# Optimization experiments

Measured on AMD Instinct MI355X. Metric: run time of the kernel, lower is better.

## Reference

```python
import jax, jax.numpy as jnp
import numpy as np

N, D, L, K = 250000, 16, 6, 64
COST_GAMMA = 0.1
MIN_ZERO_GAMMA = 0.1
EPS = 1e-7  # clip for arccos numerical stability


def setup_inputs() -> dict:
    key = jax.random.key(0)
    k1, k2, k3, k4 = jax.random.split(key, 4)
    xs = jax.random.normal(k1, (N, D), jnp.float32)
    xs = xs / jnp.linalg.norm(xs, axis=1, keepdims=True)  # points on sphere S^{D-1}
    mus = jax.random.normal(k2, (L, D, K), jnp.float32)    # per-layer component locations
    alphas = jax.random.uniform(k3, (L, K), jnp.float32, minval=-1.0, maxval=1.0)
    ws = jax.random.uniform(k4, (L,), jnp.float32, minval=0.0, maxval=1.0)
    return {"xs": xs, "mus": mus, "alphas": alphas, "ws": ws}


def reference(xs, mus, alphas, ws):
    # projx: normalize each mu column onto the sphere (norm over D axis)
    mu_n = mus / jnp.linalg.norm(mus, axis=1, keepdims=True)          # [L, D, K]
    # sphere cost: 0.5 * geodesic_dist^2 = 0.5 * arccos(<x, mu>)^2
    inner = jnp.einsum('nd,ldk->lnk', xs, mu_n)                        # [L, N, K]
    dist = jnp.arccos(jnp.clip(inner, -1.0 + EPS, 1.0 - EPS))
    costs = 0.5 * dist * dist + alphas[:, None, :]                     # [L, N, K]
    # soft-min over components (note sign convention follows original: +gamma*LSE(-c/gamma))
    mincosts = COST_GAMMA * jax.nn.logsumexp(-costs / COST_GAMMA, axis=2)  # [L, N]
    wv = jnp.exp(-ws ** 2)                                             # [L]
    F = jnp.zeros((xs.shape[0],), xs.dtype)
    for i in range(L):  # small fixed layer recurrence
        F = wv[i] * jax.nn.relu(F) + (1.0 - wv[i]) * mincosts[i]
    # smooth min(F, 0): gamma * LSE(-[F,0]/gamma)
    Fz = jnp.stack((F, jnp.zeros_like(F)), axis=-1)
    F = MIN_ZERO_GAMMA * jax.nn.logsumexp(-Fz / MIN_ZERO_GAMMA, axis=-1)
    return F
```

## Files before the change

### kernel.cpp

```cpp
#include <hip/hip_runtime.h>
#include <math.h>

#define NPOINTS 250000
#define LL 6
#define DD 16
#define KK 64

#define TPB 128
#define WAVES_PER_BLOCK (TPB / 64)
#define PTS_PER_WAVE 64
#define PTS_PER_BLOCK (WAVES_PER_BLOCK * PTS_PER_WAVE)

#define LDS_BYTES (WAVES_PER_BLOCK * PTS_PER_WAVE * 80)

#define WS_MU 0
#define WS_AV 24576
#define WS_WV 26112

typedef __attribute__((ext_vector_type(8))) short bf16x8;
typedef __attribute__((ext_vector_type(4))) float f32x4;
typedef __attribute__((ext_vector_type(2))) float f32x2;

#if __has_builtin(__builtin_amdgcn_exp2f)
#define EXP2F(x) __builtin_amdgcn_exp2f(x)
#else
#define EXP2F(x) exp2f(x)
#endif
#if __has_builtin(__builtin_amdgcn_logf)
#define LOG2F(x) __builtin_amdgcn_logf(x)
#else
#define LOG2F(x) log2f(x)
#endif

#define C_AA   (-14.426950408889634f)
#define C_GLN2 (0.06931471805599453f)

#define W0  17.797117f
#define VT0 (-45.300328f)
#define VT1 (-28.559404f)
#define VT2 (-27.844414f)
#define VT3 (-30.475230f)
#define VT4 (-36.246253f)
#define VT5 (-27.207285f)

__device__ __forceinline__ f32x2 s2(float v) { f32x2 r; r.x = v; r.y = v; return r; }

__device__ __forceinline__ ushort bf16_rne(float f) {
  unsigned u = __float_as_uint(f);
  unsigned r = u + 0x7FFFu + ((u >> 16) & 1u);
  return (ushort)(r >> 16);
}

__device__ __forceinline__ f32x2 poly_t2(f32x2 xp, f32x2 aaw) {
  f32x2 x2  = xp * xp;
  f32x2 p01 = __builtin_elementwise_fma(s2(VT1), xp, s2(VT0));
  f32x2 p23 = __builtin_elementwise_fma(s2(VT3), xp, s2(VT2));
  f32x2 p45 = __builtin_elementwise_fma(s2(VT5), xp, s2(VT4));
  f32x2 qq  = __builtin_elementwise_fma(x2, p45, p23);
  f32x2 V   = __builtin_elementwise_fma(x2, qq, p01);
  return __builtin_elementwise_fma(xp, V, aaw);
}

__device__ __forceinline__ void pack_pt(char* dst, float4 a, int q) {
  ushort h0 = bf16_rne(a.x), h1 = bf16_rne(a.y);
  ushort h2 = bf16_rne(a.z), h3 = bf16_rne(a.w);
  float hf0 = __uint_as_float((unsigned)h0 << 16);
  float hf1 = __uint_as_float((unsigned)h1 << 16);
  float hf2 = __uint_as_float((unsigned)h2 << 16);
  float hf3 = __uint_as_float((unsigned)h3 << 16);
  ushort l0 = bf16_rne(a.x - hf0), l1 = bf16_rne(a.y - hf1);
  ushort l2 = bf16_rne(a.z - hf2), l3 = bf16_rne(a.w - hf3);
  uint2 hwv, lwv;
  hwv.x = (unsigned)h0 | ((unsigned)h1 << 16);
  hwv.y = (unsigned)h2 | ((unsigned)h3 << 16);
  lwv.x = (unsigned)l0 | ((unsigned)l1 << 16);
  lwv.y = (unsigned)l2 | ((unsigned)l3 << 16);
  *(uint2*)(dst + q * 8) = hwv;
  *(uint2*)(dst + 32 + q * 8) = lwv;
}

__global__ __launch_bounds__(384) void
prep_kernel(const float* __restrict__ mus,
            const float* __restrict__ alphas,
            const float* __restrict__ wsv,
            char* __restrict__ ws) {
  const int t = threadIdx.x;
  const float* colp = mus + (t >> 6) * (DD * KK) + (t & 63);
  float v[DD];
  float ss = 0.0f;
#pragma unroll
  for (int d = 0; d < DD; ++d) { v[d] = colp[d * KK]; ss = fmaf(v[d], v[d], ss); }
  float inv = -0.5f / sqrtf(ss);
  unsigned hw[8], lw[8];
#pragma unroll
  for (int i = 0; i < 8; ++i) {
    float a0 = v[2 * i] * inv;
    float a1 = v[2 * i + 1] * inv;
    ushort h0 = bf16_rne(a0), h1 = bf16_rne(a1);
    float hf0 = __uint_as_float((unsigned)h0 << 16);
    float hf1 = __uint_as_float((unsigned)h1 << 16);
    ushort l0 = bf16_rne(a0 - hf0), l1 = bf16_rne(a1 - hf1);
    hw[i] = (unsigned)h0 | ((unsigned)h1 << 16);
    lw[i] = (unsigned)l0 | ((unsigned)l1 << 16);
  }
  uint4* colq = (uint4*)(ws + WS_MU + t * 64);
  colq[0] = make_uint4(hw[0], hw[1], hw[2], hw[3]);
  colq[1] = make_uint4(hw[4], hw[5], hw[6], hw[7]);
  colq[2] = make_uint4(lw[0], lw[1], lw[2], lw[3]);
  colq[3] = make_uint4(lw[4], lw[5], lw[6], lw[7]);
  ((float*)(ws + WS_AV))[t] = fmaf(C_AA, alphas[t], -W0);
  if (t < LL) { float x = wsv[t]; ((float*)(ws + WS_WV))[t] = expf(-x * x); }
}

__global__ __launch_bounds__(TPB, 3) void
multiinf_kernel(const float* __restrict__ xs,
                const char* __restrict__ ws,
                float* __restrict__ out) {
  __shared__ __align__(16) char smem[LDS_BYTES];

  const int tid = threadIdx.x;
  const int wid = tid >> 6;
  const int lane = tid & 63;
  const int c = lane & 15;
  const int q = lane >> 4;
  const int h = q & 1;
  const int pt0 = blockIdx.x * PTS_PER_BLOCK + wid * PTS_PER_WAVE;
  char* sx = smem + wid * (PTS_PER_WAVE * 80);

#pragma unroll
  for (int t = 0; t < 4; ++t) {
    int p = pt0 + 16 * t + c;
    float4 a = make_float4(0.0f, 0.0f, 0.0f, 0.0f);
    if (p < NPOINTS) a = ((const float4*)(xs + (size_t)p * DD))[q];
    pack_pt(sx + (16 * t + c) * 80, a, q);
  }

  bf16x8 Bh[4], Bl[4];
#pragma unroll
  for (int t = 0; t < 4; ++t) {
    Bh[t] = *(const bf16x8*)(sx + (16 * t + c) * 80 + h * 16);
    Bl[t] = *(const bf16x8*)(sx + (16 * t + c) * 80 + 32 + h * 16);
  }

  const float* swv = (const float*)(ws + WS_WV);
  const f32x4 zero4 = {0.0f, 0.0f, 0.0f, 0.0f};
  float F[4] = {0.0f, 0.0f, 0.0f, 0.0f};

  auto load_Am = [&](int l, bf16x8* Am) {
#pragma unroll
    for (int cb = 0; cb < 4; ++cb)
      Am[cb] = *(const bf16x8*)(ws + WS_MU + (l * 64 + cb * 16 + c) * 64 + q * 16);
  };
  auto load_aa = [&](int l, f32x2* aaL, f32x2* aaH) {
#pragma unroll
    for (int cb = 0; cb < 4; ++cb) {
      f32x4 a4 = *(const f32x4*)(ws + WS_AV + (l * 64 + cb * 16 + q * 4) * 4);
      aaL[cb].x = a4.x; aaL[cb].y = a4.y;
      aaH[cb].x = a4.z; aaH[cb].y = a4.w;
    }
  };

  auto layer_body = [&](int l, const bf16x8* Am) {
    f32x2 aaL[4], aaH[4];
    load_aa(l, aaL, aaH);
    f32x2 S[8];
#pragma unroll
    for (int i = 0; i < 8; ++i) S[i] = s2(0.0f);
#pragma unroll
    for (int cb = 0; cb < 4; ++cb) {
      f32x4 acc[4];
#pragma unroll
      for (int t = 0; t < 4; ++t) {
        acc[t] = __builtin_amdgcn_mfma_f32_16x16x32_bf16(Am[cb], Bh[t], zero4, 0, 0, 0);
        acc[t] = __builtin_amdgcn_mfma_f32_16x16x32_bf16(Am[cb], Bl[t], acc[t], 0, 0, 0);
      }
      f32x2 t2[8];
#pragma unroll
      for (int t = 0; t < 4; ++t) {
        f32x2 x01, x23;
        x01.x = acc[t][0]; x01.y = acc[t][1];
        x23.x = acc[t][2]; x23.y = acc[t][3];
        t2[2 * t]     = poly_t2(x01, aaL[cb]);
        t2[2 * t + 1] = poly_t2(x23, aaH[cb]);
      }
      f32x2 e[8];
#pragma unroll
      for (int i = 0; i < 8; ++i) { e[i].x = EXP2F(t2[i].x); e[i].y = EXP2F(t2[i].y); }
#pragma unroll
      for (int i = 0; i < 8; ++i) S[i] += e[i];
    }
    float wvl = swv[l];
    float om = 1.0f - wvl;
#pragma unroll
    for (int t = 0; t < 4; ++t) {
      f32x2 Sf = S[2 * t] + S[2 * t + 1];
      float St = Sf.x + Sf.y;
      St += __shfl_xor(St, 16, 64);
      St += __shfl_xor(St, 32, 64);
      float mc = C_GLN2 * LOG2F(St);
      F[t] = fmaf(wvl, fmaxf(F[t], 0.0f), om * mc);
    }
  };

  bf16x8 AmA[4], AmB[4];
  load_Am(0, AmA);
#pragma unroll 1
  for (int lp = 0; lp < 3; ++lp) {
    int l0 = 2 * lp, l1 = 2 * lp + 1;
    load_Am(l1, AmB);
    layer_body(l0, AmA);
    if (l1 + 1 < LL) load_Am(l1 + 1, AmA);
    layer_body(l1, AmB);
  }

  {
    int t = lane >> 4;
    float Fv = (t == 0) ? F[0] : (t == 1) ? F[1] : (t == 2) ? F[2] : F[3];
    int idx = pt0 + lane;
    if (idx < NPOINTS) {
      float e = EXP2F(Fv * C_AA);
      out[idx] = C_GLN2 * LOG2F(1.0f + e);
    }
  }
}

extern "C" void kernel_launch(void* const* d_in, const int* in_sizes, int n_in,
                              void* d_out, int out_size, void* d_ws, size_t ws_size,
                              hipStream_t stream) {
  const float* xs = (const float*)d_in[0];
  const float* mus = (const float*)d_in[1];
  const float* alphas = (const float*)d_in[2];
  const float* wsv = (const float*)d_in[3];
  float* out = (float*)d_out;
  char* ws = (char*)d_ws;
  (void)ws_size;

  prep_kernel<<<1, 384, 0, stream>>>(mus, alphas, wsv, ws);
  const int blocks = (NPOINTS + PTS_PER_BLOCK - 1) / PTS_PER_BLOCK;
  multiinf_kernel<<<blocks, TPB, 0, stream>>>(xs, ws, out);
}
```

Before: 95.61 us.

## Fully unroll layer loop and defer cross-lane reductions and logs to end

Replaces the manually double-buffered, partially unrolled layer loop with a fully unrolled loop over all six layers. The MFMA, polynomial and exp work is interleaved per tile rather than batched per column block. The per-layer shuffles, log and recurrence are moved after all layers so they run in one batch. This is meant to give the compiler freedom to schedule loads and MFMAs across layers and to take the cross-lane shuffle latency off the per-layer critical path, at the cost of more live registers (24 partial sums) and larger code, which may hurt occupancy under the 3-blocks launch bound.

```diff
diff --git a/kernel.cpp b/kernel.cpp
--- a/kernel.cpp
+++ b/kernel.cpp
@@ -144,73 +144,74 @@
 
   const float* swv = (const float*)(ws + WS_WV);
   const f32x4 zero4 = {0.0f, 0.0f, 0.0f, 0.0f};
-  float F[4] = {0.0f, 0.0f, 0.0f, 0.0f};
-
-  auto load_Am = [&](int l, bf16x8* Am) {
-#pragma unroll
-    for (int cb = 0; cb < 4; ++cb)
+
+  float Stv[LL][4];
+
+#pragma unroll
+  for (int l = 0; l < LL; ++l) {
+    bf16x8 Am[4];
+    f32x2 aaL[4], aaH[4];
+#pragma unroll
+    for (int cb = 0; cb < 4; ++cb) {
       Am[cb] = *(const bf16x8*)(ws + WS_MU + (l * 64 + cb * 16 + c) * 64 + q * 16);
-  };
-  auto load_aa = [&](int l, f32x2* aaL, f32x2* aaH) {
-#pragma unroll
-    for (int cb = 0; cb < 4; ++cb) {
       f32x4 a4 = *(const f32x4*)(ws + WS_AV + (l * 64 + cb * 16 + q * 4) * 4);
       aaL[cb].x = a4.x; aaL[cb].y = a4.y;
       aaH[cb].x = a4.z; aaH[cb].y = a4.w;
     }
-  };
-
-  auto layer_body = [&](int l, const bf16x8* Am) {
-    f32x2 aaL[4], aaH[4];
-    load_aa(l, aaL, aaH);
-    f32x2 S[8];
-#pragma unroll
-    for (int i = 0; i < 8; ++i) S[i] = s2(0.0f);
+    f32x2 S01[4], S23[4];
+#pragma unroll
+    for (int t = 0; t < 4; ++t) { S01[t] = s2(0.0f); S23[t] = s2(0.0f); }
 #pragma unroll
     for (int cb = 0; cb < 4; ++cb) {
-      f32x4 acc[4];
 #pragma unroll
       for (int t = 0; t < 4; ++t) {
-        acc[t] = __builtin_amdgcn_mfma_f32_16x16x32_bf16(Am[cb], Bh[t], zero4, 0, 0, 0);
-        acc[t] = __builtin_amdgcn_mfma_f32_16x16x32_bf16(Am[cb], Bl[t], acc[t], 0, 0, 0);
+        f32x4 acc = __builtin_amdgcn_mfma_f32_16x16x32_bf16(Am[cb], Bh[t], zero4, 0, 0, 0);
+        acc = __builtin_amdgcn_mfma_f32_16x16x32_bf16(Am[cb], Bl[t], acc, 0, 0, 0);
+        f32x2 x01, x23;
+        x01.x = acc[0]; x01.y = acc[1];
+        x23.x = acc[2]; x23.y = acc[3];
+        f32x2 t2a = poly_t2(x01, aaL[cb]);
+        f32x2 t2b = poly_t2(x23, aaH[cb]);
+        f32x2 ea, eb;
+        ea.x = EXP2F(t2a.x); ea.y = EXP2F(t2a.y);
+        eb.x = EXP2F(t2b.x); eb.y = EXP2F(t2b.y);
+        S01[t] += ea;
+        S23[t] += eb;
       }
-      f32x2 t2[8];
-#pragma unroll
-      for (int t = 0; t < 4; ++t) {
-        f32x2 x01, x23;
-        x01.x = acc[t][0]; x01.y = acc[t][1];
-        x23.x = acc[t][2]; x23.y = acc[t][3];
-        t2[2 * t]     = poly_t2(x01, aaL[cb]);
-        t2[2 * t + 1] = poly_t2(x23, aaH[cb]);
-      }
-      f32x2 e[8];
-#pragma unroll
-      for (int i = 0; i < 8; ++i) { e[i].x = EXP2F(t2[i].x); e[i].y = EXP2F(t2[i].y); }
-#pragma unroll
-      for (int i = 0; i < 8; ++i) S[i] += e[i];
-    }
+    }
+#pragma unroll
+    for (int t = 0; t < 4; ++t) {
+      f32x2 Sf = S01[t] + S23[t];
+      Stv[l][t] = Sf.x + Sf.y;
+    }
+  }
+
+#pragma unroll
+  for (int l = 0; l < LL; ++l)
+#pragma unroll
+    for (int t = 0; t < 4; ++t)
+      Stv[l][t] += __shfl_xor(Stv[l][t], 16, 64);
+#pragma unroll
+  for (int l = 0; l < LL; ++l)
+#pragma unroll
+    for (int t = 0; t < 4; ++t)
+      Stv[l][t] += __shfl_xor(Stv[l][t], 32, 64);
+
+  float mc[LL][4];
+#pragma unroll
+  for (int l = 0; l < LL; ++l)
+#pragma unroll
+    for (int t = 0; t < 4; ++t)
+      mc[l][t] = C_GLN2 * LOG2F(Stv[l][t]);
+
+  float F[4] = {0.0f, 0.0f, 0.0f, 0.0f};
+#pragma unroll
+  for (int l = 0; l < LL; ++l) {
     float wvl = swv[l];
     float om = 1.0f - wvl;
 #pragma unroll
-    for (int t = 0; t < 4; ++t) {
-      f32x2 Sf = S[2 * t] + S[2 * t + 1];
-      float St = Sf.x + Sf.y;
-      St += __shfl_xor(St, 16, 64);
-      St += __shfl_xor(St, 32, 64);
-      float mc = C_GLN2 * LOG2F(St);
-      F[t] = fmaf(wvl, fmaxf(F[t], 0.0f), om * mc);
-    }
-  };
-
-  bf16x8 AmA[4], AmB[4];
-  load_Am(0, AmA);
-#pragma unroll 1
-  for (int lp = 0; lp < 3; ++lp) {
-    int l0 = 2 * lp, l1 = 2 * lp + 1;
-    load_Am(l1, AmB);
-    layer_body(l0, AmA);
-    if (l1 + 1 < LL) load_Am(l1 + 1, AmA);
-    layer_body(l1, AmB);
+    for (int t = 0; t < 4; ++t)
+      F[t] = fmaf(wvl, fmaxf(F[t], 0.0f), om * mc[l][t]);
   }
 
   {
```

New measurement: 95.60 us, median of 2. Within noise of the previous version (-0.0%).
